# Kernel tuning notes

Measured on AMD Instinct MI355X. Metric: run time of the kernel, lower is better.

The kernel has to match this reference:

```python
import jax, jax.numpy as jnp
import numpy as np

B, S = 2, 2048
DIM_IN, DIM_OUT, NUM_HEADS, DIM_QK = 1024, 128, 16, 128


def setup_inputs() -> dict:
    key = jax.random.key(0)
    k0, k1, k2, k3 = jax.random.split(key, 4)
    x = jax.random.normal(k0, (B, S, DIM_IN), jnp.float32)
    mask = jax.random.bernoulli(k1, 0.1, (B, S))  # True = masked-out token
    # xavier-normal-ish scales (exact init values are irrelevant for correctness)
    std_in = float(np.sqrt(2.0 / (NUM_HEADS * DIM_QK + DIM_IN * DIM_QK)))
    proj_in = jax.random.normal(k2, (DIM_IN, NUM_HEADS, 2 * DIM_QK + DIM_OUT), jnp.float32) * std_in
    v_bias = jnp.zeros((NUM_HEADS, DIM_OUT), jnp.float32)
    std_out = float(np.sqrt(2.0 / (DIM_OUT * DIM_OUT + NUM_HEADS * DIM_OUT)))
    proj_out = jax.random.normal(k3, (NUM_HEADS, DIM_OUT, DIM_OUT), jnp.float32) * std_out
    proj_out_bias = jnp.zeros((DIM_OUT,), jnp.float32)
    return {"x": x, "mask": mask, "proj_in": proj_in, "v_bias": v_bias,
            "proj_out": proj_out, "proj_out_bias": proj_out_bias}


def _rotary(t):
    # t: [z, s, h, d]; GPT-NeoX style rotary as in the torch Rotary module
    d = t.shape[-1]
    half = -(-d // 2)  # ceil(d/2), matches torch.arange(0,-1,-2/d)
    freq_half = 10000.0 ** (jnp.arange(half, dtype=jnp.float32) * (-2.0 / d))
    freq = jnp.concatenate([freq_half, freq_half[: half - d % 2]])  # length d
    pos = jnp.arange(t.shape[1], dtype=jnp.float32)
    ang = pos[:, None] * freq[None, :]             # [s, d]
    cos = jnp.cos(ang)[None, :, None, :]
    sin = jnp.sin(ang)[None, :, None, :]
    x1, x2 = jnp.split(t, 2, axis=-1)
    rot = jnp.concatenate([-x2, x1], axis=-1)
    return t * cos + rot * sin


def _inf_cube(t):
    return t ** 3


def reference(x, mask, proj_in, v_bias, proj_out, proj_out_bias):
    qkv = jnp.einsum('zki,iho->zkho', x, proj_in)
    q, k, v = jnp.split(qkv, [DIM_QK, 2 * DIM_QK], axis=-1)
    q = _rotary(q)
    k = _rotary(k)
    scores = jnp.einsum('zqha,zkha->zqkh', q, k) / jnp.sqrt(jnp.float32(DIM_QK))
    # dual mask: row (query) OR column (key) masked -> -inf
    m = jnp.logical_or(mask[:, :, None, None], mask[:, None, :, None])  # [z,q,k,1]
    scores = jnp.where(m, -jnp.inf, scores)
    attn = jnp.nan_to_num(jax.nn.softmax(scores, axis=2))  # softmax over k; nan rows -> 0
    o = jnp.einsum('zqkh,zkhx->zqhx', attn, v + v_bias[None, None])
    out = jnp.einsum('zqhx,hxy->zqy', _inf_cube(o), proj_out) + proj_out_bias[None, None]
    return _inf_cube(out)
```

## Files before the change

kernel.cpp:

```cpp
#include <hip/hip_runtime.h>
#include <math.h>

#define BZ 2
#define SQ 2048
#define DIN 1024
#define HH 16
#define NT 6144
#define MROWS 4096
#define KOUT 2048
#define KSPLIT 8

typedef unsigned short u16t;
typedef unsigned int u32t;
typedef __attribute__((ext_vector_type(8))) short bf16x8;
typedef __attribute__((ext_vector_type(4))) float f32x4;

__device__ __forceinline__ float cubef(float x) { return x * x * x; }

__device__ __forceinline__ u16t f2bf(float f) {
    u32t b = __float_as_uint(f);
    b += 0x7FFFu + ((b >> 16) & 1u);
    return (u16t)(b >> 16);
}
__device__ __forceinline__ float bf2f(u16t u) { return __uint_as_float(((u32t)u) << 16); }
__device__ __forceinline__ u32t pk2(float a, float b) {
    return (u32t)f2bf(a) | ((u32t)f2bf(b) << 16);
}

#if __has_builtin(__builtin_amdgcn_exp2f)
#define EXP2(x) __builtin_amdgcn_exp2f(x)
#else
#define EXP2(x) exp2f(x)
#endif

__device__ __forceinline__ void load_lds16(const void* g, void* l) {
    __builtin_amdgcn_global_load_lds((const __attribute__((address_space(1))) void*)g,
                                     (__attribute__((address_space(3))) void*)l, 16, 0, 0);
}

__global__ __launch_bounds__(256) void bf16_x(const float* __restrict__ x,
                                              u16t* __restrict__ xb) {
    const size_t idx = ((size_t)blockIdx.x * 256 + threadIdx.x) * 8;
    float4 f0 = *(const float4*)&x[idx];
    float4 f1 = *(const float4*)&x[idx + 4];
    u32t h[4];
    h[0] = pk2(f0.x, f0.y); h[1] = pk2(f0.z, f0.w);
    h[2] = pk2(f1.x, f1.y); h[3] = pk2(f1.z, f1.w);
    *(uint4*)&xb[idx] = *(uint4*)&h[0];
}

__global__ __launch_bounds__(256) void rope_table(float* __restrict__ tab) {
    const int idx = blockIdx.x * 256 + threadIdx.x;
    const int s = idx >> 6, d = idx & 63;
    float f = expf(-0.14391156831212788f * (float)d);
    float sn, cs;
    sincosf((float)s * f, &sn, &cs);
    ((float2*)tab)[idx] = make_float2(cs, sn);
}

__global__ __launch_bounds__(256) void transpose_w(const float* __restrict__ W,
                                                   u16t* __restrict__ Th) {
    __shared__ float tile[64][68];
    const int n0 = blockIdx.x * 64;
    const int k0 = blockIdx.y * 64;
    const int t = threadIdx.x;
    {
        const int r = t >> 4, c = (t & 15) * 4;
        #pragma unroll
        for (int p = 0; p < 4; p++) {
            float4 v = *(const float4*)&W[(size_t)(k0 + r + p * 16) * NT + n0 + c];
            *(float4*)&tile[r + p * 16][c] = v;
        }
    }
    __syncthreads();
    const int nr = t >> 2;
    const int kc = (t & 3) * 16;
    u32t hi[8];
    #pragma unroll
    for (int j = 0; j < 8; j++)
        hi[j] = pk2(tile[kc + 2 * j][nr], tile[kc + 2 * j + 1][nr]);
    size_t ob = (size_t)(n0 + nr) * DIN + k0 + kc;
    *(uint4*)&Th[ob]     = *(uint4*)&hi[0];
    *(uint4*)&Th[ob + 8] = *(uint4*)&hi[4];
}

__global__ __launch_bounds__(256) void transpose_w2(const float* __restrict__ W,
                                                    u16t* __restrict__ Th) {
    __shared__ float tile[64][68];
    const int n0 = blockIdx.x * 64;
    const int k0 = blockIdx.y * 64;
    const int t = threadIdx.x;
    {
        const int r = t >> 4, c = (t & 15) * 4;
        #pragma unroll
        for (int p = 0; p < 4; p++) {
            float4 v = *(const float4*)&W[(size_t)(k0 + r + p * 16) * 128 + n0 + c];
            *(float4*)&tile[r + p * 16][c] = v;
        }
    }
    __syncthreads();
    const int nr = t >> 2;
    const int kc = (t & 3) * 16;
    u32t hi[8];
    #pragma unroll
    for (int j = 0; j < 8; j++)
        hi[j] = pk2(tile[kc + 2 * j][nr], tile[kc + 2 * j + 1][nr]);
    size_t ob = (size_t)(n0 + nr) * KOUT + k0 + kc;
    *(uint4*)&Th[ob]     = *(uint4*)&hi[0];
    *(uint4*)&Th[ob + 8] = *(uint4*)&hi[4];
}

#define QSC 0.12751744f

#define GQ_STAGE(TI) do {                                                  \
    const int _k0 = (TI) * 32;                                             \
    const int _bb = ((TI) & 3) * 8192;                                     \
    load_lds16(aPtr + _k0,     &smem[_bb + wbase]);                        \
    load_lds16(aPtr + _k0 + 8, &smem[_bb + wbase + 1024]);                 \
    load_lds16(bPtr + _k0,     &smem[_bb + 4096 + wbase]);                 \
    load_lds16(bPtr + _k0 + 8, &smem[_bb + 4096 + wbase + 1024]);          \
} while (0)

#define GQ_COMPUTE(TI) do {                                                \
    const int _bb = ((TI) & 3) * 8192;                                     \
    bf16x8 ah[4], bh[4];                                                   \
    _Pragma("unroll")                                                      \
    for (int mt = 0; mt < 4; mt++)                                         \
        ah[mt] = *(const bf16x8*)&smem[_bb + quad * 1024 + (wm + mt * 16 + l15) * 8]; \
    _Pragma("unroll")                                                      \
    for (int nt = 0; nt < 4; nt++)                                         \
        bh[nt] = *(const bf16x8*)&smem[_bb + 4096 + quad * 1024 + (wn + nt * 16 + l15) * 8]; \
    __builtin_amdgcn_s_setprio(1);                                         \
    _Pragma("unroll")                                                      \
    for (int mt = 0; mt < 4; mt++)                                         \
        _Pragma("unroll")                                                  \
        for (int nt = 0; nt < 4; nt++)                                     \
            acc[mt][nt] = __builtin_amdgcn_mfma_f32_16x16x32_bf16(ah[mt], bh[nt], acc[mt][nt], 0, 0, 0); \
    __builtin_amdgcn_s_setprio(0);                                         \
} while (0)

#define GQ_WAITBAR(N) do {                                                 \
    asm volatile("s_waitcnt vmcnt(" #N ")" ::: "memory");                  \
    __builtin_amdgcn_s_barrier();                                          \
    __builtin_amdgcn_sched_barrier(0);                                     \
} while (0)

__global__ __launch_bounds__(256, 2) void gemm_qkv6(const u16t* __restrict__ Ah,
                                                    const u16t* __restrict__ Bh,
                                                    const float* __restrict__ vb,
                                                    const float* __restrict__ ropetab,
                                                    u16t* __restrict__ QB,
                                                    u16t* __restrict__ KB,
                                                    u16t* __restrict__ VTh) {
    __shared__ __align__(16) u16t smem[32768];

    const int t = threadIdx.x;
    const int lane = t & 63, wid = t >> 6;
    const int quad = lane >> 4, l15 = lane & 15;
    const int wm = (wid & 1) * 64;
    const int wn = (wid >> 1) * 64;

    const int f = blockIdx.y * 48 + blockIdx.x;
    const int L = (f & 7) * 192 + (f >> 3);
    const int rect = L / 48, rrem = L - rect * 48;
    const int tileI = (rect & 7) * 6 + rrem % 6;
    const int rowIdx = (rect >> 3) * 8 + rrem / 6;
    const int h = tileI / 3, t3 = tileI - h * 3;
    const int colBase = tileI * 128;
    const int rowBase = rowIdx * 128;
    const int sm = t & 127;
    const int skh = t >> 7;

    f32x4 acc[4][4];
    #pragma unroll
    for (int i = 0; i < 4; i++)
        #pragma unroll
        for (int j = 0; j < 4; j++) acc[i][j] = (f32x4){0.f, 0.f, 0.f, 0.f};

    const u16t* aPtr = Ah + (size_t)(rowBase + sm) * DIN + skh * 16;
    const u16t* bPtr = Bh + (size_t)(colBase + sm) * DIN + skh * 16;
    const int wbase = (wid >> 1) * 2048 + (wid & 1) * 512;

    GQ_STAGE(0);
    GQ_STAGE(1);
    for (int i = 0; i < 30; i++) {
        GQ_STAGE(i + 2);
        GQ_WAITBAR(8);
        GQ_COMPUTE(i);
    }
    GQ_WAITBAR(4);
    GQ_COMPUTE(30);
    GQ_WAITBAR(0);
    GQ_COMPUTE(31);
    __syncthreads();

    const int z = rowBase >> 11;
    const int s0local = rowBase & 2047;
    const size_t zh = (size_t)(z * 16 + h);
    u16t* tl = smem;

    if (t3 == 2) {
        #pragma unroll
        for (int nt = 0; nt < 4; nt++) {
            float bbv = vb[h * 128 + wn + nt * 16 + l15];
            #pragma unroll
            for (int mt = 0; mt < 4; mt++)
                #pragma unroll
                for (int r = 0; r < 4; r++)
                    tl[(wm + mt * 16 + quad * 4 + r) * 136 + wn + nt * 16 + l15] =
                        f2bf(acc[mt][nt][r] + bbv);
        }
    } else {
        #pragma unroll
        for (int nt = 0; nt < 4; nt++)
            #pragma unroll
            for (int mt = 0; mt < 4; mt++)
                #pragma unroll
                for (int r = 0; r < 4; r++)
                    tl[(wm + mt * 16 + quad * 4 + r) * 136 + wn + nt * 16 + l15] =
                        f2bf(acc[mt][nt][r]);
    }
    __syncthreads();

    if (t3 != 2) {
        u16t* dstQK = (t3 ? KB : QB) + zh * 262144;
        const float sc = t3 ? 1.0f : QSC;
        const int rr = t >> 2;
        const int ch = (t & 3) << 4;
        #pragma unroll
        for (int half = 0; half < 2; half++) {
            const int row = rr + half * 64;
            const int s = s0local + row;
            const u16t* trow = &tl[row * 136];
            uint4 X1  = *(const uint4*)&trow[ch];
            uint4 X1b = *(const uint4*)&trow[ch + 8];
            uint4 X2  = *(const uint4*)&trow[ch + 64];
            uint4 X2b = *(const uint4*)&trow[ch + 72];
            u32t A_[8] = {X1.x, X1.y, X1.z, X1.w, X1b.x, X1b.y, X1b.z, X1b.w};
            u32t B_[8] = {X2.x, X2.y, X2.z, X2.w, X2b.x, X2b.y, X2b.z, X2b.w};
            u32t OA[8], OB[8];
            const float4* tb = (const float4*)&ropetab[(size_t)s * 128 + ch * 2];
            #pragma unroll
            for (int p = 0; p < 8; p++) {
                float4 tt = tb[p];
                float cs0 = tt.x * sc, sn0 = tt.y * sc;
                float cs1 = tt.z * sc, sn1 = tt.w * sc;
                float x1a = bf2f((u16t)(A_[p] & 0xFFFFu)), x1b = bf2f((u16t)(A_[p] >> 16));
                float x2a = bf2f((u16t)(B_[p] & 0xFFFFu)), x2b = bf2f((u16t)(B_[p] >> 16));
                OA[p] = pk2(x1a * cs0 - x2a * sn0, x1b * cs1 - x2b * sn1);
                OB[p] = pk2(x2a * cs0 + x1a * sn0, x2b * cs1 + x1b * sn1);
            }
            u16t* d0 = dstQK + (size_t)s * 128 + ch;
            *(uint4*)d0        = make_uint4(OA[0], OA[1], OA[2], OA[3]);
            *(uint4*)(d0 + 8)  = make_uint4(OA[4], OA[5], OA[6], OA[7]);
            *(uint4*)(d0 + 64) = make_uint4(OB[0], OB[1], OB[2], OB[3]);
            *(uint4*)(d0 + 72) = make_uint4(OB[4], OB[5], OB[6], OB[7]);
        }
    } else {
        u16t* dstV = VTh + zh * 262144 + (size_t)(s0local >> 5) * 4096;
        const int d = t & 127;
        const int g0 = t >> 7;
        #pragma unroll
        for (int gg = 0; gg < 2; gg++) {
            const int g = g0 + 2 * gg;
            const u16t* col = &tl[(g * 32) * 136 + d];
            u32t H[16];
            #pragma unroll
            for (int m = 0; m < 16; m++) {
                u32t lo = col[m * 136];
                u32t hi = col[(m + 16) * 136];
                H[m] = lo | (hi << 16);
            }
            u16t* dv = dstV + (size_t)g * 4096 + d * 32;
            *(uint4*)&dv[0]  = *(uint4*)&H[0];
            *(uint4*)&dv[8]  = *(uint4*)&H[4];
            *(uint4*)&dv[16] = *(uint4*)&H[8];
            *(uint4*)&dv[24] = *(uint4*)&H[12];
        }
    }
}

__global__ __launch_bounds__(256, 2) void attn_kernel9(const u16t* __restrict__ QB,
                                                       const u16t* __restrict__ KB,
                                                       const u16t* __restrict__ VTh,
                                                       const int* __restrict__ mask,
                                                       u16t* __restrict__ O3b) {
    const int blk = blockIdx.x;
    const int qt = blk & 15;
    const int h  = (blk >> 4) & 15;
    const int z  = blk >> 8;
    const int t  = threadIdx.x;
    const int lane = t & 63, wid = t >> 6;
    const int quad = lane >> 4, l15 = lane & 15;

    __shared__ __align__(16) u16t ks[2][32 * 136];
    __shared__ __align__(16) u16t vth[2][128 * 40];
    __shared__ __align__(16) u16t wlb[128 * 40];
    __shared__ int km[2][32];

    const int q0 = qt * 128;
    const size_t zh = (size_t)(z * 16 + h);
    const u16t* qb  = QB  + zh * 262144;
    const u16t* kb  = KB  + zh * 262144;
    const u16t* vhg = VTh + zh * 262144;

    bf16x8 qf[2][4];
    #pragma unroll
    for (int i = 0; i < 2; i++)
        #pragma unroll
        for (int kk = 0; kk < 4; kk++)
            qf[i][kk] = *(const bf16x8*)(qb + (size_t)(q0 + 16 * (2 * wid + i) + l15) * 128 + kk * 32 + quad * 8);

    int4 qm4[2];
    #pragma unroll
    for (int i = 0; i < 2; i++)
        qm4[i] = *(const int4*)&mask[z * SQ + q0 + 16 * (2 * wid + i) + 4 * quad];
    const int qmr[2][4] = {{qm4[0].x, qm4[0].y, qm4[0].z, qm4[0].w},
                           {qm4[1].x, qm4[1].y, qm4[1].z, qm4[1].w}};
    int rowoff[2];
    #pragma unroll
    for (int i = 0; i < 2; i++) rowoff[i] = (16 * (2 * wid + i) + 4 * quad) * 40;

    const int srow = t >> 3, sco = (t & 7) * 16;
    const int sdd = t >> 1, sk0 = (t & 1) * 16;

    uint4 ka, kb2, va, vb2;
    int kmv = 0;
    {
        ka  = *(const uint4*)(kb + t * 16);
        kb2 = *(const uint4*)(kb + t * 16 + 8);
        va  = *(const uint4*)(vhg + t * 16);
        vb2 = *(const uint4*)(vhg + t * 16 + 8);
        if (t < 32) kmv = mask[z * SQ + t];
    }

    f32x4 acc[2][8];
    #pragma unroll
    for (int i = 0; i < 2; i++)
        #pragma unroll
        for (int d = 0; d < 8; d++) acc[i][d] = (f32x4){0.f, 0.f, 0.f, 0.f};
    float dsum[2][4] = {{0.f, 0.f, 0.f, 0.f}, {0.f, 0.f, 0.f, 0.f}};

    for (int it = 0; it < 64; it++) {
        const int buf = it & 1;
        *(uint4*)&ks[buf][srow * 136 + sco]     = ka;
        *(uint4*)&ks[buf][srow * 136 + sco + 8] = kb2;
        *(uint4*)&vth[buf][sdd * 40 + sk0]      = va;
        *(uint4*)&vth[buf][sdd * 40 + sk0 + 8]  = vb2;
        if (t < 32) km[buf][t] = kmv;

        __syncthreads();

        {
            const int ktn = (it < 63) ? (it + 1) * 32 : it * 32;
            const u16t* src = kb + (size_t)ktn * 128 + t * 16;
            ka  = *(const uint4*)(src);
            kb2 = *(const uint4*)(src + 8);
            const u16t* srch = vhg + (size_t)(ktn >> 5) * 4096 + t * 16;
            va  = *(const uint4*)(srch);
            vb2 = *(const uint4*)(srch + 8);
            if (t < 32) kmv = mask[z * SQ + ktn + t];
        }

        f32x4 s4[2][2];
        #pragma unroll
        for (int i = 0; i < 2; i++)
            #pragma unroll
            for (int n = 0; n < 2; n++) s4[i][n] = (f32x4){0.f, 0.f, 0.f, 0.f};
        __builtin_amdgcn_s_setprio(1);
        #pragma unroll
        for (int kk = 0; kk < 4; kk++) {
            bf16x8 kf0 = *(const bf16x8*)&ks[buf][l15 * 136 + kk * 32 + quad * 8];
            bf16x8 kf1 = *(const bf16x8*)&ks[buf][(16 + l15) * 136 + kk * 32 + quad * 8];
            s4[0][0] = __builtin_amdgcn_mfma_f32_16x16x32_bf16(qf[0][kk], kf0, s4[0][0], 0, 0, 0);
            s4[0][1] = __builtin_amdgcn_mfma_f32_16x16x32_bf16(qf[0][kk], kf1, s4[0][1], 0, 0, 0);
            s4[1][0] = __builtin_amdgcn_mfma_f32_16x16x32_bf16(qf[1][kk], kf0, s4[1][0], 0, 0, 0);
            s4[1][1] = __builtin_amdgcn_mfma_f32_16x16x32_bf16(qf[1][kk], kf1, s4[1][1], 0, 0, 0);
        }
        __builtin_amdgcn_s_setprio(0);
        {
            int colm0 = km[buf][l15], colm1 = km[buf][16 + l15];
            #pragma unroll
            for (int i = 0; i < 2; i++)
                #pragma unroll
                for (int r = 0; r < 4; r++) {
                    float w0 = colm0 ? 0.f : EXP2(s4[i][0][r]);
                    float w1 = colm1 ? 0.f : EXP2(s4[i][1][r]);
                    dsum[i][r] += w0 + w1;
                    u32t pkw;
                    asm("v_cvt_pk_bf16_f32 %0, %1, %2" : "=v"(pkw) : "v"(w0), "v"(w1));
                    *(u32t*)&wlb[rowoff[i] + r * 40 + 2 * l15] = pkw;
                }
        }
        bf16x8 pa[2];
        #pragma unroll
        for (int i = 0; i < 2; i++)
            pa[i] = *(const bf16x8*)&wlb[(16 * (2 * wid + i) + l15) * 40 + quad * 8];
        __builtin_amdgcn_s_setprio(1);
        #pragma unroll
        for (int dt = 0; dt < 8; dt++) {
            bf16x8 vh = *(const bf16x8*)&vth[buf][(16 * dt + l15) * 40 + quad * 8];
            acc[0][dt] = __builtin_amdgcn_mfma_f32_16x16x32_bf16(pa[0], vh, acc[0][dt], 0, 0, 0);
            acc[1][dt] = __builtin_amdgcn_mfma_f32_16x16x32_bf16(pa[1], vh, acc[1][dt], 0, 0, 0);
        }
        __builtin_amdgcn_s_setprio(0);
    }

    #pragma unroll
    for (int i = 0; i < 2; i++)
        #pragma unroll
        for (int r = 0; r < 4; r++) {
            float v = dsum[i][r];
            v += __shfl_xor(v, 1);
            v += __shfl_xor(v, 2);
            v += __shfl_xor(v, 4);
            v += __shfl_xor(v, 8);
            dsum[i][r] = v;
        }

    #pragma unroll
    for (int i = 0; i < 2; i++)
        #pragma unroll
        for (int r = 0; r < 4; r++) {
            int row = 16 * (2 * wid + i) + 4 * quad + r;
            float inv = (qmr[i][r] || !(dsum[i][r] > 0.f)) ? 0.f : 1.f / dsum[i][r];
            u16t* dst = O3b + (size_t)(z * SQ + q0 + row) * KOUT + h * 128;
            #pragma unroll
            for (int dt = 0; dt < 8; dt++)
                dst[16 * dt + l15] = f2bf(cubef(acc[i][dt][r] * inv));
        }
}

__global__ __launch_bounds__(256, 2) void final_gemm4(const u16t* __restrict__ Ab,
                                                      const u16t* __restrict__ Bh,
                                                      float* __restrict__ part) {
    __shared__ __align__(16) u16t smem[32768];

    const int t = threadIdx.x;
    const int lane = t & 63, wid = t >> 6;
    const int quad = lane >> 4, l15 = lane & 15;
    const int wm = (wid & 1) * 64;
    const int wn = (wid >> 1) * 64;
    const int rowBase = blockIdx.x * 128;
    const int kBase   = blockIdx.y * (KOUT / KSPLIT);
    const int sm = t & 127;
    const int skh = t >> 7;

    f32x4 acc[4][4];
    #pragma unroll
    for (int i = 0; i < 4; i++)
        #pragma unroll
        for (int j = 0; j < 4; j++) acc[i][j] = (f32x4){0.f, 0.f, 0.f, 0.f};

    const u16t* aPtr = Ab + (size_t)(rowBase + sm) * KOUT + kBase + skh * 16;
    const u16t* bPtr = Bh + (size_t)sm * KOUT + kBase + skh * 16;
    const int wbase = (wid >> 1) * 2048 + (wid & 1) * 512;

    GQ_STAGE(0);
    GQ_STAGE(1);
    for (int i = 0; i < 6; i++) {
        GQ_STAGE(i + 2);
        GQ_WAITBAR(8);
        GQ_COMPUTE(i);
    }
    GQ_WAITBAR(4);
    GQ_COMPUTE(6);
    GQ_WAITBAR(0);
    GQ_COMPUTE(7);

    float* pbase = part + (size_t)blockIdx.y * ((size_t)MROWS * 128);
    #pragma unroll
    for (int mt = 0; mt < 4; mt++)
        #pragma unroll
        for (int nt = 0; nt < 4; nt++) {
            int col = wn + nt * 16 + l15;
            #pragma unroll
            for (int r = 0; r < 4; r++) {
                int row = rowBase + wm + mt * 16 + quad * 4 + r;
                pbase[(size_t)row * 128 + col] = acc[mt][nt][r];
            }
        }
}

__global__ __launch_bounds__(256) void reduce_bias_cube(const float* __restrict__ part,
                                                        const float* __restrict__ bias,
                                                        float* __restrict__ out) {
    const int idx = (blockIdx.x * 256 + threadIdx.x) * 4;
    float4 s = {0.f, 0.f, 0.f, 0.f};
    #pragma unroll
    for (int p = 0; p < KSPLIT; p++) {
        float4 v = *(const float4*)&part[(size_t)p * ((size_t)MROWS * 128) + idx];
        s.x += v.x; s.y += v.y; s.z += v.z; s.w += v.w;
    }
    float4 b = *(const float4*)&bias[idx & 127];
    float4 r;
    r.x = cubef(s.x + b.x);
    r.y = cubef(s.y + b.y);
    r.z = cubef(s.z + b.z);
    r.w = cubef(s.w + b.w);
    *(float4*)&out[idx] = r;
}

extern "C" void kernel_launch(void* const* d_in, const int* in_sizes, int n_in,
                              void* d_out, int out_size, void* d_ws, size_t ws_size,
                              hipStream_t stream) {
    const float* x        = (const float*)d_in[0];
    const int*   mask     = (const int*)d_in[1];
    const float* proj_in  = (const float*)d_in[2];
    const float* v_bias   = (const float*)d_in[3];
    const float* proj_out = (const float*)d_in[4];
    const float* po_bias  = (const float*)d_in[5];
    float* out = (float*)d_out;

    u16t* QB  = (u16t*)d_ws;
    u16t* KB  = QB + (size_t)8388608;
    u16t* VTh = KB + (size_t)8388608;
    u16t* xb  = VTh + (size_t)8388608;
    u16t* O3b = xb + (size_t)4194304;
    u16t* pTh = O3b;
    float* ropetab = (float*)(O3b + (size_t)6291456);
    u16t* WTh = QB;
    float* partials = (float*)(WTh + (size_t)128 * KOUT);

    bf16_x<<<(MROWS * DIN) / (256 * 8), 256, 0, stream>>>(x, xb);
    rope_table<<<(SQ * 64) / 256, 256, 0, stream>>>(ropetab);
    transpose_w<<<dim3(NT / 64, DIN / 64), 256, 0, stream>>>(proj_in, pTh);
    gemm_qkv6<<<dim3(48, MROWS / 128), 256, 0, stream>>>(xb, pTh, v_bias, ropetab, QB, KB, VTh);
    attn_kernel9<<<BZ * HH * (SQ / 128), 256, 0, stream>>>(QB, KB, VTh, mask, O3b);
    transpose_w2<<<dim3(2, KOUT / 64), 256, 0, stream>>>(proj_out, WTh);
    final_gemm4<<<dim3(MROWS / 128, KSPLIT), 256, 0, stream>>>(O3b, WTh, partials);
    reduce_bias_cube<<<(MROWS * 128) / (256 * 4), 256, 0, stream>>>(partials, po_bias, out);
}
```

Before: 300.6 us.

## Enlarge QKV GEMM tiles to 256x256 with 512-thread blocks

Replaces the 128x128-tile QKV projection GEMM with a 256x256-tile version using 8 waves per block, each wave computing a 128x64 sub-tile. The epilogue now handles two head-tile halves in sequence for the RoPE/V-transpose writes. The larger tiles raise arithmetic intensity and cut redundant global/L2 loads. In exchange they need 128KB of LDS, more accumulator registers per thread and fewer blocks (384), which can lower occupancy and leave parts of the GPU idle in the tail.

New measurement: 383.6 us. +27.6%, slower.

```diff
diff --git a/kernel.cpp b/kernel.cpp
--- a/kernel.cpp
+++ b/kernel.cpp
@@ -111,6 +111,331 @@
 }
 
 #define QSC 0.12751744f
+
+#define GQ_WAITBAR(N) do {                                                 \
+    asm volatile("s_waitcnt vmcnt(" #N ")" ::: "memory");                  \
+    __builtin_amdgcn_s_barrier();                                          \
+    __builtin_amdgcn_sched_barrier(0);                                     \
+} while (0)
+
+#define GQ2_STAGE(TI) do {                                                 \
+    const int _k0 = (TI) * 32;                                             \
+    const int _bb = ((TI) & 3) * 16384;                                    \
+    load_lds16(aP + _k0,      &smem[_bb + wid * 512]);                     \
+    load_lds16(aP + _k0 + 16, &smem[_bb + wid * 512 + 4096]);              \
+    load_lds16(bP + _k0,      &smem[_bb + 8192 + wid * 512]);              \
+    load_lds16(bP + _k0 + 16, &smem[_bb + 8192 + wid * 512 + 4096]);       \
+} while (0)
+
+#define GQ2_COMPUTE(TI) do {                                               \
+    const int _bb = ((TI) & 3) * 16384;                                    \
+    bf16x8 ah[8], bh[4];                                                   \
+    _Pragma("unroll")                                                      \
+    for (int mt = 0; mt < 8; mt++)                                         \
+        ah[mt] = *(const bf16x8*)&smem[_bb + quad * 2048 + (wrow + mt * 16 + l15) * 8]; \
+    _Pragma("unroll")                                                      \
+    for (int nt = 0; nt < 4; nt++)                                         \
+        bh[nt] = *(const bf16x8*)&smem[_bb + 8192 + quad * 2048 + (wcol + nt * 16 + l15) * 8]; \
+    __builtin_amdgcn_s_setprio(1);                                         \
+    _Pragma("unroll")                                                      \
+    for (int mt = 0; mt < 8; mt++)                                         \
+        _Pragma("unroll")                                                  \
+        for (int nt = 0; nt < 4; nt++)                                     \
+            acc[mt][nt] = __builtin_amdgcn_mfma_f32_16x16x32_bf16(ah[mt], bh[nt], acc[mt][nt], 0, 0, 0); \
+    __builtin_amdgcn_s_setprio(0);                                         \
+} while (0)
+
+__global__ __launch_bounds__(512, 2) void gemm_qkv7(const u16t* __restrict__ Ah,
+                                                    const u16t* __restrict__ Bh,
+                                                    const float* __restrict__ vb,
+                                                    const float* __restrict__ ropetab,
+                                                    u16t* __restrict__ QB,
+                                                    u16t* __restrict__ KB,
+                                                    u16t* __restrict__ VTh) {
+    __shared__ __align__(16) u16t smem[65536];
+
+    const int t = threadIdx.x;
+    const int lane = t & 63, wid = t >> 6;
+    const int quad = lane >> 4, l15 = lane & 15;
+    const int wrow = (wid >> 2) * 128;
+    const int wcol = (wid & 3) * 64;
+
+    const int f = blockIdx.y * 24 + blockIdx.x;
+    const int xcd = f & 7, lidx = f >> 3;
+    const int gx = (xcd & 3) * 6 + lidx % 6;
+    const int gy = (xcd >> 2) * 8 + lidx / 6;
+    const int rowBase = gy * 256;
+    const int colBase = gx * 256;
+
+    f32x4 acc[8][4];
+    #pragma unroll
+    for (int i = 0; i < 8; i++)
+        #pragma unroll
+        for (int j = 0; j < 4; j++) acc[i][j] = (f32x4){0.f, 0.f, 0.f, 0.f};
+
+    const int srow = (wid & 3) * 64 + lane;
+    const int kcf  = (wid >> 2) * 8;
+    const u16t* aP = Ah + (size_t)(rowBase + srow) * DIN + kcf;
+    const u16t* bP = Bh + (size_t)(colBase + srow) * DIN + kcf;
+
+    GQ2_STAGE(0);
+    GQ2_STAGE(1);
+    for (int i = 0; i < 30; i++) {
+        GQ2_STAGE(i + 2);
+        GQ_WAITBAR(8);
+        GQ2_COMPUTE(i);
+    }
+    GQ_WAITBAR(4);
+    GQ2_COMPUTE(30);
+    GQ_WAITBAR(0);
+    GQ2_COMPUTE(31);
+    __syncthreads();
+
+    const int z = rowBase >> 11;
+    const int s0local = rowBase & 2047;
+    u16t* tl = smem;
+
+    for (int hf = 0; hf < 2; hf++) {
+        const int tileIdx = 2 * gx + hf;
+        const int hh = tileIdx / 3, t3 = tileIdx - hh * 3;
+        const size_t zh = (size_t)(z * 16 + hh);
+
+        if (((wid >> 1) & 1) == hf) {
+            const int cb = (wid & 1) * 64;
+            if (t3 == 2) {
+                #pragma unroll
+                for (int nt = 0; nt < 4; nt++) {
+                    float bbv = vb[hh * 128 + cb + nt * 16 + l15];
+                    #pragma unroll
+                    for (int mt = 0; mt < 8; mt++)
+                        #pragma unroll
+                        for (int r = 0; r < 4; r++)
+                            tl[(wrow + mt * 16 + quad * 4 + r) * 136 + cb + nt * 16 + l15] =
+                                f2bf(acc[mt][nt][r] + bbv);
+                }
+            } else {
+                #pragma unroll
+                for (int nt = 0; nt < 4; nt++)
+                    #pragma unroll
+                    for (int mt = 0; mt < 8; mt++)
+                        #pragma unroll
+                        for (int r = 0; r < 4; r++)
+                            tl[(wrow + mt * 16 + quad * 4 + r) * 136 + cb + nt * 16 + l15] =
+                                f2bf(acc[mt][nt][r]);
+            }
+        }
+        __syncthreads();
+
+        if (t3 != 2) {
+            u16t* dstQK = (t3 ? KB : QB) + zh * 262144;
+            const float sc = t3 ? 1.0f : QSC;
+            const int rr = t >> 1;
+            const int cbase = (t & 1) * 32;
+            const int s = s0local + rr;
+            const u16t* trow = &tl[rr * 136];
+            #pragma unroll
+            for (int cc = 0; cc < 2; cc++) {
+                const int c0 = cbase + cc * 16;
+                uint4 X1  = *(const uint4*)&trow[c0];
+                uint4 X1b = *(const uint4*)&trow[c0 + 8];
+                uint4 X2  = *(const uint4*)&trow[c0 + 64];
+                uint4 X2b = *(const uint4*)&trow[c0 + 72];
+                u32t A_[8] = {X1.x, X1.y, X1.z, X1.w, X1b.x, X1b.y, X1b.z, X1b.w};
+                u32t B_[8] = {X2.x, X2.y, X2.z, X2.w, X2b.x, X2b.y, X2b.z, X2b.w};
+                u32t OA[8], OB[8];
+                const float4* tb = (const float4*)&ropetab[(size_t)s * 128 + c0 * 2];
+                #pragma unroll
+                for (int p = 0; p < 8; p++) {
+                    float4 tt = tb[p];
+                    float cs0 = tt.x * sc, sn0 = tt.y * sc;
+                    float cs1 = tt.z * sc, sn1 = tt.w * sc;
+                    float x1a = bf2f((u16t)(A_[p] & 0xFFFFu)), x1b = bf2f((u16t)(A_[p] >> 16));
+                    float x2a = bf2f((u16t)(B_[p] & 0xFFFFu)), x2b = bf2f((u16t)(B_[p] >> 16));
+                    OA[p] = pk2(x1a * cs0 - x2a * sn0, x1b * cs1 - x2b * sn1);
+                    OB[p] = pk2(x2a * cs0 + x1a * sn0, x2b * cs1 + x1b * sn1);
+                }
+                u16t* d0 = dstQK + (size_t)s * 128 + c0;
+                *(uint4*)d0        = make_uint4(OA[0], OA[1], OA[2], OA[3]);
+                *(uint4*)(d0 + 8)  = make_uint4(OA[4], OA[5], OA[6], OA[7]);
+                *(uint4*)(d0 + 64) = make_uint4(OB[0], OB[1], OB[2], OB[3]);
+                *(uint4*)(d0 + 72) = make_uint4(OB[4], OB[5], OB[6], OB[7]);
+            }
+        } else {
+            u16t* dstV = VTh + zh * 262144 + (size_t)(s0local >> 5) * 4096;
+            const int d = t & 127;
+            const int g0 = t >> 7;
+            #pragma unroll
+            for (int gg = 0; gg < 2; gg++) {
+                const int g = g0 + 4 * gg;
+                const u16t* col = &tl[(g * 32) * 136 + d];
+                u32t H[16];
+                #pragma unroll
+                for (int m = 0; m < 16; m++) {
+                    u32t lo = col[m * 136];
+                    u32t hi = col[(m + 16) * 136];
+                    H[m] = lo | (hi << 16);
+                }
+                u16t* dv = dstV + (size_t)g * 4096 + d * 32;
+                *(uint4*)&dv[0]  = *(uint4*)&H[0];
+                *(uint4*)&dv[8]  = *(uint4*)&H[4];
+                *(uint4*)&dv[16] = *(uint4*)&H[8];
+                *(uint4*)&dv[24] = *(uint4*)&H[12];
+            }
+        }
+        __syncthreads();
+    }
+}
+
+__global__ __launch_bounds__(256, 2) void attn_kernel9(const u16t* __restrict__ QB,
+                                                       const u16t* __restrict__ KB,
+                                                       const u16t* __restrict__ VTh,
+                                                       const int* __restrict__ mask,
+                                                       u16t* __restrict__ O3b) {
+    const int blk = blockIdx.x;
+    const int qt = blk & 15;
+    const int h  = (blk >> 4) & 15;
+    const int z  = blk >> 8;
+    const int t  = threadIdx.x;
+    const int lane = t & 63, wid = t >> 6;
+    const int quad = lane >> 4, l15 = lane & 15;
+
+    __shared__ __align__(16) u16t ks[2][32 * 136];
+    __shared__ __align__(16) u16t vth[2][128 * 40];
+    __shared__ __align__(16) u16t wlb[128 * 40];
+    __shared__ int km[2][32];
+
+    const int q0 = qt * 128;
+    const size_t zh = (size_t)(z * 16 + h);
+    const u16t* qb  = QB  + zh * 262144;
+    const u16t* kb  = KB  + zh * 262144;
+    const u16t* vhg = VTh + zh * 262144;
+
+    bf16x8 qf[2][4];
+    #pragma unroll
+    for (int i = 0; i < 2; i++)
+        #pragma unroll
+        for (int kk = 0; kk < 4; kk++)
+            qf[i][kk] = *(const bf16x8*)(qb + (size_t)(q0 + 16 * (2 * wid + i) + l15) * 128 + kk * 32 + quad * 8);
+
+    int4 qm4[2];
+    #pragma unroll
+    for (int i = 0; i < 2; i++)
+        qm4[i] = *(const int4*)&mask[z * SQ + q0 + 16 * (2 * wid + i) + 4 * quad];
+    const int qmr[2][4] = {{qm4[0].x, qm4[0].y, qm4[0].z, qm4[0].w},
+                           {qm4[1].x, qm4[1].y, qm4[1].z, qm4[1].w}};
+    int rowoff[2];
+    #pragma unroll
+    for (int i = 0; i < 2; i++) rowoff[i] = (16 * (2 * wid + i) + 4 * quad) * 40;
+
+    const int srow = t >> 3, sco = (t & 7) * 16;
+    const int sdd = t >> 1, sk0 = (t & 1) * 16;
+
+    uint4 ka, kb2, va, vb2;
+    int kmv = 0;
+    {
+        ka  = *(const uint4*)(kb + t * 16);
+        kb2 = *(const uint4*)(kb + t * 16 + 8);
+        va  = *(const uint4*)(vhg + t * 16);
+        vb2 = *(const uint4*)(vhg + t * 16 + 8);
+        if (t < 32) kmv = mask[z * SQ + t];
+    }
+
+    f32x4 acc[2][8];
+    #pragma unroll
+    for (int i = 0; i < 2; i++)
+        #pragma unroll
+        for (int d = 0; d < 8; d++) acc[i][d] = (f32x4){0.f, 0.f, 0.f, 0.f};
+    float dsum[2][4] = {{0.f, 0.f, 0.f, 0.f}, {0.f, 0.f, 0.f, 0.f}};
+
+    for (int it = 0; it < 64; it++) {
+        const int buf = it & 1;
+        *(uint4*)&ks[buf][srow * 136 + sco]     = ka;
+        *(uint4*)&ks[buf][srow * 136 + sco + 8] = kb2;
+        *(uint4*)&vth[buf][sdd * 40 + sk0]      = va;
+        *(uint4*)&vth[buf][sdd * 40 + sk0 + 8]  = vb2;
+        if (t < 32) km[buf][t] = kmv;
+
+        __syncthreads();
+
+        {
+            const int ktn = (it < 63) ? (it + 1) * 32 : it * 32;
+            const u16t* src = kb + (size_t)ktn * 128 + t * 16;
+            ka  = *(const uint4*)(src);
+            kb2 = *(const uint4*)(src + 8);
+            const u16t* srch = vhg + (size_t)(ktn >> 5) * 4096 + t * 16;
+            va  = *(const uint4*)(srch);
+            vb2 = *(const uint4*)(srch + 8);
+            if (t < 32) kmv = mask[z * SQ + ktn + t];
+        }
+
+        f32x4 s4[2][2];
+        #pragma unroll
+        for (int i = 0; i < 2; i++)
+            #pragma unroll
+            for (int n = 0; n < 2; n++) s4[i][n] = (f32x4){0.f, 0.f, 0.f, 0.f};
+        __builtin_amdgcn_s_setprio(1);
+        #pragma unroll
+        for (int kk = 0; kk < 4; kk++) {
+            bf16x8 kf0 = *(const bf16x8*)&ks[buf][l15 * 136 + kk * 32 + quad * 8];
+            bf16x8 kf1 = *(const bf16x8*)&ks[buf][(16 + l15) * 136 + kk * 32 + quad * 8];
+            s4[0][0] = __builtin_amdgcn_mfma_f32_16x16x32_bf16(qf[0][kk], kf0, s4[0][0], 0, 0, 0);
+            s4[0][1] = __builtin_amdgcn_mfma_f32_16x16x32_bf16(qf[0][kk], kf1, s4[0][1], 0, 0, 0);
+            s4[1][0] = __builtin_amdgcn_mfma_f32_16x16x32_bf16(qf[1][kk], kf0, s4[1][0], 0, 0, 0);
+            s4[1][1] = __builtin_amdgcn_mfma_f32_16x16x32_bf16(qf[1][kk], kf1, s4[1][1], 0, 0, 0);
+        }
+        __builtin_amdgcn_s_setprio(0);
+        {
+            int colm0 = km[buf][l15], colm1 = km[buf][16 + l15];
+            #pragma unroll
+            for (int i = 0; i < 2; i++)
+                #pragma unroll
+                for (int r = 0; r < 4; r++) {
+                    float w0 = colm0 ? 0.f : EXP2(s4[i][0][r]);
+                    float w1 = colm1 ? 0.f : EXP2(s4[i][1][r]);
+                    dsum[i][r] += w0 + w1;
+                    u32t pkw;
+                    asm("v_cvt_pk_bf16_f32 %0, %1, %2" : "=v"(pkw) : "v"(w0), "v"(w1));
+                    *(u32t*)&wlb[rowoff[i] + r * 40 + 2 * l15] = pkw;
+                }
+        }
+        bf16x8 pa[2];
+        #pragma unroll
+        for (int i = 0; i < 2; i++)
+            pa[i] = *(const bf16x8*)&wlb[(16 * (2 * wid + i) + l15) * 40 + quad * 8];
+        __builtin_amdgcn_s_setprio(1);
+        #pragma unroll
+        for (int dt = 0; dt < 8; dt++) {
+            bf16x8 vh = *(const bf16x8*)&vth[buf][(16 * dt + l15) * 40 + quad * 8];
+            acc[0][dt] = __builtin_amdgcn_mfma_f32_16x16x32_bf16(pa[0], vh, acc[0][dt], 0, 0, 0);
+            acc[1][dt] = __builtin_amdgcn_mfma_f32_16x16x32_bf16(pa[1], vh, acc[1][dt], 0, 0, 0);
+        }
+        __builtin_amdgcn_s_setprio(0);
+    }
+
+    #pragma unroll
+    for (int i = 0; i < 2; i++)
+        #pragma unroll
+        for (int r = 0; r < 4; r++) {
+            float v = dsum[i][r];
+            v += __shfl_xor(v, 1);
+            v += __shfl_xor(v, 2);
+            v += __shfl_xor(v, 4);
+            v += __shfl_xor(v, 8);
+            dsum[i][r] = v;
+        }
+
+    #pragma unroll
+    for (int i = 0; i < 2; i++)
+        #pragma unroll
+        for (int r = 0; r < 4; r++) {
+            int row = 16 * (2 * wid + i) + 4 * quad + r;
+            float inv = (qmr[i][r] || !(dsum[i][r] > 0.f)) ? 0.f : 1.f / dsum[i][r];
+            u16t* dst = O3b + (size_t)(z * SQ + q0 + row) * KOUT + h * 128;
+            #pragma unroll
+            for (int dt = 0; dt < 8; dt++)
+                dst[16 * dt + l15] = f2bf(cubef(acc[i][dt][r] * inv));
+        }
+}
 
 #define GQ_STAGE(TI) do {                                                  \
     const int _k0 = (TI) * 32;                                             \
@@ -139,298 +464,6 @@
     __builtin_amdgcn_s_setprio(0);                                         \
 } while (0)
 
-#define GQ_WAITBAR(N) do {                                                 \
-    asm volatile("s_waitcnt vmcnt(" #N ")" ::: "memory");                  \
-    __builtin_amdgcn_s_barrier();                                          \
-    __builtin_amdgcn_sched_barrier(0);                                     \
-} while (0)
-
-__global__ __launch_bounds__(256, 2) void gemm_qkv6(const u16t* __restrict__ Ah,
-                                                    const u16t* __restrict__ Bh,
-                                                    const float* __restrict__ vb,
-                                                    const float* __restrict__ ropetab,
-                                                    u16t* __restrict__ QB,
-                                                    u16t* __restrict__ KB,
-                                                    u16t* __restrict__ VTh) {
-    __shared__ __align__(16) u16t smem[32768];
-
-    const int t = threadIdx.x;
-    const int lane = t & 63, wid = t >> 6;
-    const int quad = lane >> 4, l15 = lane & 15;
-    const int wm = (wid & 1) * 64;
-    const int wn = (wid >> 1) * 64;
-
-    const int f = blockIdx.y * 48 + blockIdx.x;
-    const int L = (f & 7) * 192 + (f >> 3);
-    const int rect = L / 48, rrem = L - rect * 48;
-    const int tileI = (rect & 7) * 6 + rrem % 6;
-    const int rowIdx = (rect >> 3) * 8 + rrem / 6;
-    const int h = tileI / 3, t3 = tileI - h * 3;
-    const int colBase = tileI * 128;
-    const int rowBase = rowIdx * 128;
-    const int sm = t & 127;
-    const int skh = t >> 7;
-
-    f32x4 acc[4][4];
-    #pragma unroll
-    for (int i = 0; i < 4; i++)
-        #pragma unroll
-        for (int j = 0; j < 4; j++) acc[i][j] = (f32x4){0.f, 0.f, 0.f, 0.f};
-
-    const u16t* aPtr = Ah + (size_t)(rowBase + sm) * DIN + skh * 16;
-    const u16t* bPtr = Bh + (size_t)(colBase + sm) * DIN + skh * 16;
-    const int wbase = (wid >> 1) * 2048 + (wid & 1) * 512;
-
-    GQ_STAGE(0);
-    GQ_STAGE(1);
-    for (int i = 0; i < 30; i++) {
-        GQ_STAGE(i + 2);
-        GQ_WAITBAR(8);
-        GQ_COMPUTE(i);
-    }
-    GQ_WAITBAR(4);
-    GQ_COMPUTE(30);
-    GQ_WAITBAR(0);
-    GQ_COMPUTE(31);
-    __syncthreads();
-
-    const int z = rowBase >> 11;
-    const int s0local = rowBase & 2047;
-    const size_t zh = (size_t)(z * 16 + h);
-    u16t* tl = smem;
-
-    if (t3 == 2) {
-        #pragma unroll
-        for (int nt = 0; nt < 4; nt++) {
-            float bbv = vb[h * 128 + wn + nt * 16 + l15];
-            #pragma unroll
-            for (int mt = 0; mt < 4; mt++)
-                #pragma unroll
-                for (int r = 0; r < 4; r++)
-                    tl[(wm + mt * 16 + quad * 4 + r) * 136 + wn + nt * 16 + l15] =
-                        f2bf(acc[mt][nt][r] + bbv);
-        }
-    } else {
-        #pragma unroll
-        for (int nt = 0; nt < 4; nt++)
-            #pragma unroll
-            for (int mt = 0; mt < 4; mt++)
-                #pragma unroll
-                for (int r = 0; r < 4; r++)
-                    tl[(wm + mt * 16 + quad * 4 + r) * 136 + wn + nt * 16 + l15] =
-                        f2bf(acc[mt][nt][r]);
-    }
-    __syncthreads();
-
-    if (t3 != 2) {
-        u16t* dstQK = (t3 ? KB : QB) + zh * 262144;
-        const float sc = t3 ? 1.0f : QSC;
-        const int rr = t >> 2;
-        const int ch = (t & 3) << 4;
-        #pragma unroll
-        for (int half = 0; half < 2; half++) {
-            const int row = rr + half * 64;
-            const int s = s0local + row;
-            const u16t* trow = &tl[row * 136];
-            uint4 X1  = *(const uint4*)&trow[ch];
-            uint4 X1b = *(const uint4*)&trow[ch + 8];
-            uint4 X2  = *(const uint4*)&trow[ch + 64];
-            uint4 X2b = *(const uint4*)&trow[ch + 72];
-            u32t A_[8] = {X1.x, X1.y, X1.z, X1.w, X1b.x, X1b.y, X1b.z, X1b.w};
-            u32t B_[8] = {X2.x, X2.y, X2.z, X2.w, X2b.x, X2b.y, X2b.z, X2b.w};
-            u32t OA[8], OB[8];
-            const float4* tb = (const float4*)&ropetab[(size_t)s * 128 + ch * 2];
-            #pragma unroll
-            for (int p = 0; p < 8; p++) {
-                float4 tt = tb[p];
-                float cs0 = tt.x * sc, sn0 = tt.y * sc;
-                float cs1 = tt.z * sc, sn1 = tt.w * sc;
-                float x1a = bf2f((u16t)(A_[p] & 0xFFFFu)), x1b = bf2f((u16t)(A_[p] >> 16));
-                float x2a = bf2f((u16t)(B_[p] & 0xFFFFu)), x2b = bf2f((u16t)(B_[p] >> 16));
-                OA[p] = pk2(x1a * cs0 - x2a * sn0, x1b * cs1 - x2b * sn1);
-                OB[p] = pk2(x2a * cs0 + x1a * sn0, x2b * cs1 + x1b * sn1);
-            }
-            u16t* d0 = dstQK + (size_t)s * 128 + ch;
-            *(uint4*)d0        = make_uint4(OA[0], OA[1], OA[2], OA[3]);
-            *(uint4*)(d0 + 8)  = make_uint4(OA[4], OA[5], OA[6], OA[7]);
-            *(uint4*)(d0 + 64) = make_uint4(OB[0], OB[1], OB[2], OB[3]);
-            *(uint4*)(d0 + 72) = make_uint4(OB[4], OB[5], OB[6], OB[7]);
-        }
-    } else {
-        u16t* dstV = VTh + zh * 262144 + (size_t)(s0local >> 5) * 4096;
-        const int d = t & 127;
-        const int g0 = t >> 7;
-        #pragma unroll
-        for (int gg = 0; gg < 2; gg++) {
-            const int g = g0 + 2 * gg;
-            const u16t* col = &tl[(g * 32) * 136 + d];
-            u32t H[16];
-            #pragma unroll
-            for (int m = 0; m < 16; m++) {
-                u32t lo = col[m * 136];
-                u32t hi = col[(m + 16) * 136];
-                H[m] = lo | (hi << 16);
-            }
-            u16t* dv = dstV + (size_t)g * 4096 + d * 32;
-            *(uint4*)&dv[0]  = *(uint4*)&H[0];
-            *(uint4*)&dv[8]  = *(uint4*)&H[4];
-            *(uint4*)&dv[16] = *(uint4*)&H[8];
-            *(uint4*)&dv[24] = *(uint4*)&H[12];
-        }
-    }
-}
-
-__global__ __launch_bounds__(256, 2) void attn_kernel9(const u16t* __restrict__ QB,
-                                                       const u16t* __restrict__ KB,
-                                                       const u16t* __restrict__ VTh,
-                                                       const int* __restrict__ mask,
-                                                       u16t* __restrict__ O3b) {
-    const int blk = blockIdx.x;
-    const int qt = blk & 15;
-    const int h  = (blk >> 4) & 15;
-    const int z  = blk >> 8;
-    const int t  = threadIdx.x;
-    const int lane = t & 63, wid = t >> 6;
-    const int quad = lane >> 4, l15 = lane & 15;
-
-    __shared__ __align__(16) u16t ks[2][32 * 136];
-    __shared__ __align__(16) u16t vth[2][128 * 40];
-    __shared__ __align__(16) u16t wlb[128 * 40];
-    __shared__ int km[2][32];
-
-    const int q0 = qt * 128;
-    const size_t zh = (size_t)(z * 16 + h);
-    const u16t* qb  = QB  + zh * 262144;
-    const u16t* kb  = KB  + zh * 262144;
-    const u16t* vhg = VTh + zh * 262144;
-
-    bf16x8 qf[2][4];
-    #pragma unroll
-    for (int i = 0; i < 2; i++)
-        #pragma unroll
-        for (int kk = 0; kk < 4; kk++)
-            qf[i][kk] = *(const bf16x8*)(qb + (size_t)(q0 + 16 * (2 * wid + i) + l15) * 128 + kk * 32 + quad * 8);
-
-    int4 qm4[2];
-    #pragma unroll
-    for (int i = 0; i < 2; i++)
-        qm4[i] = *(const int4*)&mask[z * SQ + q0 + 16 * (2 * wid + i) + 4 * quad];
-    const int qmr[2][4] = {{qm4[0].x, qm4[0].y, qm4[0].z, qm4[0].w},
-                           {qm4[1].x, qm4[1].y, qm4[1].z, qm4[1].w}};
-    int rowoff[2];
-    #pragma unroll
-    for (int i = 0; i < 2; i++) rowoff[i] = (16 * (2 * wid + i) + 4 * quad) * 40;
-
-    const int srow = t >> 3, sco = (t & 7) * 16;
-    const int sdd = t >> 1, sk0 = (t & 1) * 16;
-
-    uint4 ka, kb2, va, vb2;
-    int kmv = 0;
-    {
-        ka  = *(const uint4*)(kb + t * 16);
-        kb2 = *(const uint4*)(kb + t * 16 + 8);
-        va  = *(const uint4*)(vhg + t * 16);
-        vb2 = *(const uint4*)(vhg + t * 16 + 8);
-        if (t < 32) kmv = mask[z * SQ + t];
-    }
-
-    f32x4 acc[2][8];
-    #pragma unroll
-    for (int i = 0; i < 2; i++)
-        #pragma unroll
-        for (int d = 0; d < 8; d++) acc[i][d] = (f32x4){0.f, 0.f, 0.f, 0.f};
-    float dsum[2][4] = {{0.f, 0.f, 0.f, 0.f}, {0.f, 0.f, 0.f, 0.f}};
-
-    for (int it = 0; it < 64; it++) {
-        const int buf = it & 1;
-        *(uint4*)&ks[buf][srow * 136 + sco]     = ka;
-        *(uint4*)&ks[buf][srow * 136 + sco + 8] = kb2;
-        *(uint4*)&vth[buf][sdd * 40 + sk0]      = va;
-        *(uint4*)&vth[buf][sdd * 40 + sk0 + 8]  = vb2;
-        if (t < 32) km[buf][t] = kmv;
-
-        __syncthreads();
-
-        {
-            const int ktn = (it < 63) ? (it + 1) * 32 : it * 32;
-            const u16t* src = kb + (size_t)ktn * 128 + t * 16;
-            ka  = *(const uint4*)(src);
-            kb2 = *(const uint4*)(src + 8);
-            const u16t* srch = vhg + (size_t)(ktn >> 5) * 4096 + t * 16;
-            va  = *(const uint4*)(srch);
-            vb2 = *(const uint4*)(srch + 8);
-            if (t < 32) kmv = mask[z * SQ + ktn + t];
-        }
-
-        f32x4 s4[2][2];
-        #pragma unroll
-        for (int i = 0; i < 2; i++)
-            #pragma unroll
-            for (int n = 0; n < 2; n++) s4[i][n] = (f32x4){0.f, 0.f, 0.f, 0.f};
-        __builtin_amdgcn_s_setprio(1);
-        #pragma unroll
-        for (int kk = 0; kk < 4; kk++) {
-            bf16x8 kf0 = *(const bf16x8*)&ks[buf][l15 * 136 + kk * 32 + quad * 8];
-            bf16x8 kf1 = *(const bf16x8*)&ks[buf][(16 + l15) * 136 + kk * 32 + quad * 8];
-            s4[0][0] = __builtin_amdgcn_mfma_f32_16x16x32_bf16(qf[0][kk], kf0, s4[0][0], 0, 0, 0);
-            s4[0][1] = __builtin_amdgcn_mfma_f32_16x16x32_bf16(qf[0][kk], kf1, s4[0][1], 0, 0, 0);
-            s4[1][0] = __builtin_amdgcn_mfma_f32_16x16x32_bf16(qf[1][kk], kf0, s4[1][0], 0, 0, 0);
-            s4[1][1] = __builtin_amdgcn_mfma_f32_16x16x32_bf16(qf[1][kk], kf1, s4[1][1], 0, 0, 0);
-        }
-        __builtin_amdgcn_s_setprio(0);
-        {
-            int colm0 = km[buf][l15], colm1 = km[buf][16 + l15];
-            #pragma unroll
-            for (int i = 0; i < 2; i++)
-                #pragma unroll
-                for (int r = 0; r < 4; r++) {
-                    float w0 = colm0 ? 0.f : EXP2(s4[i][0][r]);
-                    float w1 = colm1 ? 0.f : EXP2(s4[i][1][r]);
-                    dsum[i][r] += w0 + w1;
-                    u32t pkw;
-                    asm("v_cvt_pk_bf16_f32 %0, %1, %2" : "=v"(pkw) : "v"(w0), "v"(w1));
-                    *(u32t*)&wlb[rowoff[i] + r * 40 + 2 * l15] = pkw;
-                }
-        }
-        bf16x8 pa[2];
-        #pragma unroll
-        for (int i = 0; i < 2; i++)
-            pa[i] = *(const bf16x8*)&wlb[(16 * (2 * wid + i) + l15) * 40 + quad * 8];
-        __builtin_amdgcn_s_setprio(1);
-        #pragma unroll
-        for (int dt = 0; dt < 8; dt++) {
-            bf16x8 vh = *(const bf16x8*)&vth[buf][(16 * dt + l15) * 40 + quad * 8];
-            acc[0][dt] = __builtin_amdgcn_mfma_f32_16x16x32_bf16(pa[0], vh, acc[0][dt], 0, 0, 0);
-            acc[1][dt] = __builtin_amdgcn_mfma_f32_16x16x32_bf16(pa[1], vh, acc[1][dt], 0, 0, 0);
-        }
-        __builtin_amdgcn_s_setprio(0);
-    }
-
-    #pragma unroll
-    for (int i = 0; i < 2; i++)
-        #pragma unroll
-        for (int r = 0; r < 4; r++) {
-            float v = dsum[i][r];
-            v += __shfl_xor(v, 1);
-            v += __shfl_xor(v, 2);
-            v += __shfl_xor(v, 4);
-            v += __shfl_xor(v, 8);
-            dsum[i][r] = v;
-        }
-
-    #pragma unroll
-    for (int i = 0; i < 2; i++)
-        #pragma unroll
-        for (int r = 0; r < 4; r++) {
-            int row = 16 * (2 * wid + i) + 4 * quad + r;
-            float inv = (qmr[i][r] || !(dsum[i][r] > 0.f)) ? 0.f : 1.f / dsum[i][r];
-            u16t* dst = O3b + (size_t)(z * SQ + q0 + row) * KOUT + h * 128;
-            #pragma unroll
-            for (int dt = 0; dt < 8; dt++)
-                dst[16 * dt + l15] = f2bf(cubef(acc[i][dt][r] * inv));
-        }
-}
-
 __global__ __launch_bounds__(256, 2) void final_gemm4(const u16t* __restrict__ Ab,
                                                       const u16t* __restrict__ Bh,
                                                       float* __restrict__ part) {
@@ -525,7 +558,7 @@
     bf16_x<<<(MROWS * DIN) / (256 * 8), 256, 0, stream>>>(x, xb);
     rope_table<<<(SQ * 64) / 256, 256, 0, stream>>>(ropetab);
     transpose_w<<<dim3(NT / 64, DIN / 64), 256, 0, stream>>>(proj_in, pTh);
-    gemm_qkv6<<<dim3(48, MROWS / 128), 256, 0, stream>>>(xb, pTh, v_bias, ropetab, QB, KB, VTh);
+    gemm_qkv7<<<dim3(24, 16), 512, 0, stream>>>(xb, pTh, v_bias, ropetab, QB, KB, VTh);
     attn_kernel9<<<BZ * HH * (SQ / 128), 256, 0, stream>>>(QB, KB, VTh, mask, O3b);
     transpose_w2<<<dim3(2, KOUT / 64), 256, 0, stream>>>(proj_out, WTh);
     final_gemm4<<<dim3(MROWS / 128, KSPLIT), 256, 0, stream>>>(O3b, WTh, partials);
```
